# Performance work log

Hardware: AMD Instinct MI355X
Metric: run time of the kernel (lower is better)

## Reference

```python
import jax, jax.numpy as jnp
import numpy as np

N = 50000      # nodes
E = 800000     # edges (avg degree 16)
IN, HID, OUT = 256, 128, 64
K, ALPHA = 4, 0.0  # APPNPConv(k=4, alpha=0.0)


def setup_inputs() -> dict:
    key = jax.random.key(0)
    ks = jax.random.split(key, 5)
    features = jax.random.normal(ks[0], (N, IN), jnp.float32)
    src = jax.random.randint(ks[1], (E,), 0, N, jnp.int32)
    dst = jax.random.randint(ks[2], (E,), 0, N, jnp.int32)
    W1 = jax.random.normal(ks[3], (IN, HID), jnp.float32) / np.float32(np.sqrt(IN))
    b1 = jnp.zeros((HID,), jnp.float32)
    W3 = jax.random.normal(ks[4], (HID, OUT), jnp.float32) / np.float32(np.sqrt(HID))
    b3 = jnp.zeros((OUT,), jnp.float32)
    return dict(features=features, src=src, dst=dst, W1=W1, b1=b1, W3=W3, b3=b3)


def _sym_norms(src, dst, n):
    # D_out^{-1/2} for source side, D_in^{-1/2} for destination side (DGL norm='both')
    ones = jnp.ones((src.shape[0],), jnp.float32)
    deg_out = jax.ops.segment_sum(ones, src, num_segments=n)
    deg_in = jax.ops.segment_sum(ones, dst, num_segments=n)
    return jnp.clip(deg_out, 1.0) ** -0.5, jnp.clip(deg_in, 1.0) ** -0.5


def _prop(x, src, dst, norm_src, norm_dst):
    # x: [N, D]. Symmetric-normalized SpMM: D_in^{-1/2} A D_out^{-1/2} x
    msg = (x * norm_src[:, None])[src]                       # [E, D] gather
    agg = jax.ops.segment_sum(msg, dst, num_segments=x.shape[0])  # [N, D] scatter-add
    return agg * norm_dst[:, None]


def reference(features, src, dst, W1, b1, W3, b3):
    ns, nd = _sym_norms(src, dst, N)
    # GraphConv 1 (weight-first since in_dim > hidden_dim; math identical either way)
    h = _prop(features @ W1, src, dst, ns, nd) + b1
    # dropout is identity in eval mode (training=False)
    # APPNPConv: k=4 power-iteration steps with teleport alpha=0.0
    h0 = h
    for _ in range(K):
        h = (1.0 - ALPHA) * _prop(h, src, dst, ns, nd) + ALPHA * h0
    # GraphConv 3
    out = _prop(h @ W3, src, dst, ns, nd) + b3
    return out
```

## Files before the change

kernel.cpp:

```cpp
#include <hip/hip_runtime.h>
#include <math.h>

#define N_NODES 50000
#define N_EDGES 800000
#define DIN 256
#define DHID 128
#define DOUT 64
#define CSTRIDE 64
#define ZROW N_NODES
#define HBLOCKS 128
#define HCHUNK (N_EDGES / HBLOCKS)
#define HWORDS (N_NODES / 4)
#define SLICE ((size_t)(N_NODES + 1) * 16)
#define NGROUPS (N_NODES / 4)
#define P2BLOCKS 196

#define SB_SENT 3125
#define SB_HS (SB_SENT + HBLOCKS)
#define SB_HD (SB_HS + HBLOCKS)
#define SB_TOT (SB_HD + 66)

__global__ void k_setup(const int* __restrict__ src, const int* __restrict__ dst,
                        unsigned int* __restrict__ pS, unsigned int* __restrict__ pD,
                        unsigned int* __restrict__ csr32,
                        const float* __restrict__ W1, const float* __restrict__ b1,
                        const float* __restrict__ W3,
                        float* __restrict__ W13, float* __restrict__ bb,
                        float* __restrict__ Y0, float* __restrict__ Y1) {
    __shared__ unsigned int h[HWORDS];
    int bx = blockIdx.x, t = threadIdx.x;
    if (bx < SB_SENT) {
        unsigned int v = (unsigned int)ZROW | ((unsigned int)ZROW << 16);
        uint2 o; o.x = v; o.y = v;
        ((uint2*)csr32)[bx * 256 + t] = o;
        return;
    }
    if (bx < SB_HD) {
        const int* idx = (bx < SB_HS) ? src : dst;
        unsigned int* outp = (bx < SB_HS) ? pS : pD;
        int hb = bx - ((bx < SB_HS) ? SB_SENT : SB_HS);
        for (int w = t; w < HWORDS; w += 256) h[w] = 0u;
        __syncthreads();
        int base = hb * HCHUNK;
        for (int i = t; i < HCHUNK; i += 256) {
            int s = idx[base + i];
            atomicAdd(&h[s >> 2], 1u << ((s & 3) << 3));
        }
        __syncthreads();
        outp += (size_t)hb * HWORDS;
        for (int w = t; w < HWORDS; w += 256) outp[w] = h[w];
        return;
    }
    int vb = bx - SB_HD;
    if (vb == 65) {
        if (t < 64) {
            int qq = t >> 4, c2 = t & 15;
            Y0[(size_t)qq * SLICE + ((size_t)ZROW << 4) + c2] = 0.f;
        } else if (t < 128) {
            int t2 = t - 64;
            int qq = t2 >> 4, c2 = t2 & 15;
            Y1[(size_t)qq * SLICE + ((size_t)ZROW << 4) + c2] = 0.f;
        }
        return;
    }
    if (vb == 64) {
        if (t < DOUT) {
            float s = 0.f;
            for (int k = 0; k < DHID; ++k) s += b1[k] * W3[k * DOUT + t];
            bb[t] = s;
        }
        return;
    }
    int idx2 = vb * 256 + t;
    int i = idx2 >> 6, j = idx2 & 63;
    float s = 0.f;
    for (int k = 0; k < DHID; ++k) s += W1[i * DHID + k] * W3[k * DOUT + j];
    W13[idx2] = s;
}

__global__ void k_hpre(const unsigned int* __restrict__ pS,
                       const unsigned int* __restrict__ pD,
                       unsigned int* __restrict__ prefix,
                       float* __restrict__ ns, float* __restrict__ nd,
                       float* __restrict__ cc, int* __restrict__ mG) {
    __shared__ unsigned int sdw[64][4];
    __shared__ unsigned int sow[64][4];
    int t = threadIdx.x;
    int col = t >> 2, sub = t & 3;
    int wid = blockIdx.x * 64 + col;
    bool act = wid < HWORDS;
    unsigned int vals[32];
    unsigned int ps = 0, pd = 0;
    int b0 = sub << 5;
    if (act) {
#pragma unroll
        for (int k = 0; k < 32; ++k) {
            ps += pS[(size_t)(b0 + k) * HWORDS + wid];
            unsigned int w = pD[(size_t)(b0 + k) * HWORDS + wid];
            vals[k] = w;
            pd += w;
        }
    }
    sdw[col][sub] = pd;
    sow[col][sub] = ps;
    __syncthreads();
    if (act) {
        unsigned int base = 0;
        for (int k = 0; k < sub; ++k) base += sdw[col][k];
        unsigned int run = base;
#pragma unroll
        for (int k = 0; k < 32; ++k) {
            prefix[(size_t)(b0 + k) * HWORDS + wid] = run;
            run += vals[k];
        }
        if (sub == 0) {
            unsigned int totd = sdw[col][0] + sdw[col][1] + sdw[col][2] + sdw[col][3];
            unsigned int toto = sow[col][0] + sow[col][1] + sow[col][2] + sow[col][3];
            unsigned int di[4] = {totd & 0xffu, (totd >> 8) & 0xffu,
                                  (totd >> 16) & 0xffu, totd >> 24};
            unsigned int dov[4] = {toto & 0xffu, (toto >> 8) & 0xffu,
                                   (toto >> 16) & 0xffu, toto >> 24};
            float4 vns, vnd, vcc;
            float* pns = &vns.x; float* pnd = &vnd.x; float* pcc = &vcc.x;
            unsigned int mx = 0;
#pragma unroll
            for (int q = 0; q < 4; ++q) {
                if (di[q] > mx) mx = di[q];
                unsigned int a = dov[q] < 1u ? 1u : dov[q];
                unsigned int b = di[q] < 1u ? 1u : di[q];
                float fa = 1.0f / sqrtf((float)a);
                float fb = 1.0f / sqrtf((float)b);
                pns[q] = fa; pnd[q] = fb; pcc[q] = fa * fb;
            }
            *(float4*)(ns + (wid << 2)) = vns;
            *(float4*)(nd + (wid << 2)) = vnd;
            *(float4*)(cc + (wid << 2)) = vcc;
            int m = ((int)mx + 7) & ~7;
            mG[wid] = m > 64 ? 64 : m;
        }
    }
}

__global__ void k_fill(const int* __restrict__ src, const int* __restrict__ dst,
                       const unsigned int* __restrict__ prefix,
                       unsigned short* __restrict__ csr) {
    __shared__ unsigned int h[HWORDS];
    int t = threadIdx.x;
    const unsigned int* prow = prefix + (size_t)blockIdx.x * HWORDS;
    for (int w = t; w < HWORDS; w += 256) h[w] = prow[w];
    __syncthreads();
    int base = blockIdx.x * HCHUNK;
    for (int i = t; i < HCHUNK; i += 256) {
        int s = src[base + i], d = dst[base + i];
        int sh = (d & 3) << 3;
        unsigned int old = atomicAdd(&h[d >> 2], 1u << sh);
        int slot = (int)((old >> sh) & 0xffu);
        csr[((size_t)d << 6) + slot] = (unsigned short)s;
    }
}

__global__ void k_gemm(const float* __restrict__ X, const float* __restrict__ W13,
                       const float* __restrict__ ns, float* __restrict__ Y) {
    __shared__ float As[16][68];
    __shared__ float Bs[16][64];
    int tid = threadIdx.x;
    int tx = tid & 15, ty = tid >> 4;
    int row0 = blockIdx.x * 64;
    float acc[4][4];
#pragma unroll
    for (int i = 0; i < 4; ++i)
#pragma unroll
        for (int j = 0; j < 4; ++j) acc[i][j] = 0.f;

    int lr = tid >> 2;
    int lk = (tid & 3) << 2;
    int arow = row0 + lr;
    if (arow > N_NODES - 1) arow = N_NODES - 1;

    for (int k0 = 0; k0 < DIN; k0 += 16) {
        float4 a = *(const float4*)(X + (size_t)arow * DIN + k0 + lk);
        As[lk + 0][lr] = a.x; As[lk + 1][lr] = a.y;
        As[lk + 2][lr] = a.z; As[lk + 3][lr] = a.w;
        float4 b = *(const float4*)(W13 + (size_t)(k0 + (tid >> 4)) * DOUT + ((tid & 15) << 2));
        *(float4*)&Bs[tid >> 4][(tid & 15) << 2] = b;
        __syncthreads();
#pragma unroll
        for (int k = 0; k < 16; ++k) {
            float4 av = *(const float4*)&As[k][ty << 2];
            float4 bv = *(const float4*)&Bs[k][tx << 2];
            float ar[4] = {av.x, av.y, av.z, av.w};
            float br[4] = {bv.x, bv.y, bv.z, bv.w};
#pragma unroll
            for (int i = 0; i < 4; ++i)
#pragma unroll
                for (int j = 0; j < 4; ++j) acc[i][j] += ar[i] * br[j];
        }
        __syncthreads();
    }
    int qq = tx >> 2;
    int co = (tx & 3) << 2;
#pragma unroll
    for (int i = 0; i < 4; ++i) {
        int row = row0 + (ty << 2) + i;
        if (row < N_NODES) {
            float nsr = ns[row];
            float4 o;
            o.x = acc[i][0] * nsr; o.y = acc[i][1] * nsr;
            o.z = acc[i][2] * nsr; o.w = acc[i][3] * nsr;
            *(float4*)(Y + (size_t)qq * SLICE + ((size_t)row << 4) + co) = o;
        }
    }
}


template <int MODE>
__launch_bounds__(256, 8)
__global__ void k_spmm(const float* __restrict__ xs, float* __restrict__ ys,
                       const unsigned short* __restrict__ csr,
                       const int* __restrict__ mG,
                       const float* __restrict__ cc, const float* __restrict__ ns,
                       const float* __restrict__ nd,
                       const float* __restrict__ bb, const float* __restrict__ b3) {
    __shared__ unsigned short rows[4][256];
    int wid  = threadIdx.x >> 6;
    int lane = threadIdx.x & 63;
    int q    = (blockIdx.x & 7) >> 1;
    int half = blockIdx.x & 1;
    int g    = (blockIdx.x >> 3) * 8 + wid * 2 + half;
    if (g >= NGROUPS) return;
    int node0 = g << 2;

    int nn = lane >> 4, sl = lane & 15;
    const uint2* crow = (const uint2*)(csr + ((size_t)(node0 + nn) << 6)) + sl;
    uint2 rv = *crow;
    unsigned short* bp = &rows[wid][(sl << 4) + nn];
    bp[0]  = (unsigned short)(rv.x & 0xffffu);
    bp[4]  = (unsigned short)(rv.x >> 16);
    bp[8]  = (unsigned short)(rv.y & 0xffffu);
    bp[12] = (unsigned short)(rv.y >> 16);

    int m = __builtin_amdgcn_readfirstlane(mG[g]);

    int n = lane >> 4, e = (lane >> 2) & 3, c4 = lane & 3;
    const unsigned short* rd = &rows[wid][(e << 2) + n];
    const float* xq = xs + (size_t)q * SLICE + (c4 << 2);

    float ax = 0.f, ay = 0.f, az = 0.f, aw = 0.f;
#define LDV(T) const float4 v##T = *(const float4*)(xq + ((size_t)rd[16 * (T)] << 4))
#define ACCV(T) ax += v##T.x; ay += v##T.y; az += v##T.z; aw += v##T.w
    if (m <= 8) {
        LDV(0); LDV(1);
        ACCV(0); ACCV(1);
    } else if (m <= 16) {
        LDV(0); LDV(1); LDV(2); LDV(3);
        ACCV(0); ACCV(1); ACCV(2); ACCV(3);
    } else if (m <= 24) {
        LDV(0); LDV(1); LDV(2); LDV(3); LDV(4); LDV(5);
        ACCV(0); ACCV(1); ACCV(2); ACCV(3); ACCV(4); ACCV(5);
    } else if (m <= 32) {
        LDV(0); LDV(1); LDV(2); LDV(3); LDV(4); LDV(5); LDV(6); LDV(7);
        ACCV(0); ACCV(1); ACCV(2); ACCV(3); ACCV(4); ACCV(5); ACCV(6); ACCV(7);
    } else {
        for (int j2 = 0; j2 < m; j2 += 8) {
            int o = j2 << 2;
            const float4 a = *(const float4*)(xq + ((size_t)rd[o] << 4));
            const float4 b = *(const float4*)(xq + ((size_t)rd[o + 16] << 4));
            ax += a.x; ay += a.y; az += a.z; aw += a.w;
            ax += b.x; ay += b.y; az += b.z; aw += b.w;
        }
    }
#undef LDV
#undef ACCV
    ax += __shfl_xor(ax, 4);  ay += __shfl_xor(ay, 4);
    az += __shfl_xor(az, 4);  aw += __shfl_xor(aw, 4);
    ax += __shfl_xor(ax, 8);  ay += __shfl_xor(ay, 8);
    az += __shfl_xor(az, 8);  aw += __shfl_xor(aw, 8);

    int nodeL = node0 + n;
    int colq  = (q << 4) + (c4 << 2);
    float4 r;
    if (MODE == 0) {
        float cv = cc[nodeL], nv = ns[nodeL];
        float4 bv = *(const float4*)(bb + colq);
        r.x = cv * ax + nv * bv.x; r.y = cv * ay + nv * bv.y;
        r.z = cv * az + nv * bv.z; r.w = cv * aw + nv * bv.w;
    } else if (MODE == 1) {
        float cv = cc[nodeL];
        r.x = cv * ax; r.y = cv * ay; r.z = cv * az; r.w = cv * aw;
    } else {
        float dv = nd[nodeL];
        float4 bv = *(const float4*)(b3 + colq);
        r.x = dv * ax + bv.x; r.y = dv * ay + bv.y;
        r.z = dv * az + bv.z; r.w = dv * aw + bv.w;
    }
    if (e == 0) {
        if (MODE == 2) {
            *(float4*)(ys + ((size_t)nodeL << 6) + colq) = r;
        } else {
            *(float4*)(ys + (size_t)q * SLICE + ((size_t)nodeL << 4) + (c4 << 2)) = r;
        }
    }
}


extern "C" void kernel_launch(void* const* d_in, const int* in_sizes, int n_in,
                              void* d_out, int out_size, void* d_ws, size_t ws_size,
                              hipStream_t stream) {
    const float* X   = (const float*)d_in[0];
    const int*   src = (const int*)d_in[1];
    const int*   dst = (const int*)d_in[2];
    const float* W1  = (const float*)d_in[3];
    const float* b1  = (const float*)d_in[4];
    const float* W3  = (const float*)d_in[5];
    const float* b3  = (const float*)d_in[6];
    float* out = (float*)d_out;

    char* ws = (char*)d_ws;
    size_t off = 0;
    auto alloc = [&](size_t bytes) -> void* {
        void* p = ws + off;
        off = (off + bytes + 255) & ~(size_t)255;
        return p;
    };
    unsigned int*   pS   = (unsigned int*)alloc((size_t)HBLOCKS * HWORDS * 4);
    unsigned int*   pD   = (unsigned int*)alloc((size_t)HBLOCKS * HWORDS * 4);
    unsigned int*   pref = (unsigned int*)alloc((size_t)HBLOCKS * HWORDS * 4);
    float*          Y0   = (float*)alloc(SLICE * 4 * 4);
    float*          Y1   = (float*)alloc(SLICE * 4 * 4);
    unsigned short* csr  = (unsigned short*)alloc((size_t)N_NODES * CSTRIDE * 2);
    float*          ns   = (float*)alloc((size_t)N_NODES * 4);
    float*          nd   = (float*)alloc((size_t)N_NODES * 4);
    float*          cc   = (float*)alloc((size_t)N_NODES * 4);
    int*            mG   = (int*)alloc((size_t)NGROUPS * 4);
    float*          W13  = (float*)alloc((size_t)DIN * DOUT * 4);
    float*          bb   = (float*)alloc(DOUT * 4);

    const int sblk = 1563 * 8;

    k_setup<<<SB_TOT, 256, 0, stream>>>(src, dst, pS, pD, (unsigned int*)csr,
                                        W1, b1, W3, W13, bb, Y0, Y1);
    k_hpre<<<P2BLOCKS, 256, 0, stream>>>(pS, pD, pref, ns, nd, cc, mG);
    k_fill<<<HBLOCKS, 256, 0, stream>>>(src, dst, pref, csr);
    k_gemm<<<(N_NODES + 63) / 64, 256, 0, stream>>>(X, W13, ns, Y0);

    k_spmm<0><<<sblk, 256, 0, stream>>>(Y0, Y1, csr, mG, cc, ns, nd, bb, b3);
    k_spmm<1><<<sblk, 256, 0, stream>>>(Y1, Y0, csr, mG, cc, ns, nd, bb, b3);
    k_spmm<1><<<sblk, 256, 0, stream>>>(Y0, Y1, csr, mG, cc, ns, nd, bb, b3);
    k_spmm<1><<<sblk, 256, 0, stream>>>(Y1, Y0, csr, mG, cc, ns, nd, bb, b3);
    k_spmm<1><<<sblk, 256, 0, stream>>>(Y0, Y1, csr, mG, cc, ns, nd, bb, b3);
    k_spmm<2><<<sblk, 256, 0, stream>>>(Y1, out, csr, mG, cc, ns, nd, bb, b3);
}
```

Baseline: 293.5 us.

## Merge CSR fill and feature GEMM into one launch with 512-thread blocks

The CSR fill kernel and the X·W13 GEMM are combined into a single kernel. Block index picks the role: the first 128 blocks fill the CSR and the rest compute GEMM tiles, now 128 rows per block with 512 threads. This removes one launch and lets the two independent phases run at the same time. Both roles share a dynamic LDS allocation sized for the fill histogram (50 KB), which may reduce occupancy for the GEMM blocks.

```diff
diff --git a/kernel.cpp b/kernel.cpp
--- a/kernel.cpp
+++ b/kernel.cpp
@@ -141,53 +141,62 @@
     }
 }
 
-__global__ void k_fill(const int* __restrict__ src, const int* __restrict__ dst,
-                       const unsigned int* __restrict__ prefix,
-                       unsigned short* __restrict__ csr) {
-    __shared__ unsigned int h[HWORDS];
-    int t = threadIdx.x;
-    const unsigned int* prow = prefix + (size_t)blockIdx.x * HWORDS;
-    for (int w = t; w < HWORDS; w += 256) h[w] = prow[w];
-    __syncthreads();
-    int base = blockIdx.x * HCHUNK;
-    for (int i = t; i < HCHUNK; i += 256) {
-        int s = src[base + i], d = dst[base + i];
-        int sh = (d & 3) << 3;
-        unsigned int old = atomicAdd(&h[d >> 2], 1u << sh);
-        int slot = (int)((old >> sh) & 0xffu);
-        csr[((size_t)d << 6) + slot] = (unsigned short)s;
-    }
-}
-
-__global__ void k_gemm(const float* __restrict__ X, const float* __restrict__ W13,
-                       const float* __restrict__ ns, float* __restrict__ Y) {
-    __shared__ float As[16][68];
-    __shared__ float Bs[16][64];
-    int tid = threadIdx.x;
-    int tx = tid & 15, ty = tid >> 4;
-    int row0 = blockIdx.x * 64;
+#define MB_FILL 128
+#define MB_GEMM 391
+#define MB_TOT (MB_FILL + MB_GEMM)
+#define MID_LDS (HWORDS * 4)
+
+__global__ void k_mid(const int* __restrict__ src, const int* __restrict__ dst,
+                      const unsigned int* __restrict__ prefix,
+                      unsigned short* __restrict__ csr,
+                      const float* __restrict__ X, const float* __restrict__ W13,
+                      const float* __restrict__ ns, float* __restrict__ Y) {
+    extern __shared__ char smem[];
+    int bx = blockIdx.x, t = threadIdx.x;
+    if (bx < MB_FILL) {
+        unsigned int* h = (unsigned int*)smem;
+        const unsigned int* prow = prefix + (size_t)bx * HWORDS;
+        for (int w = t; w < HWORDS; w += 512) h[w] = prow[w];
+        __syncthreads();
+        int base = bx * HCHUNK;
+        for (int i = t; i < HCHUNK; i += 512) {
+            int s = src[base + i], d = dst[base + i];
+            int sh = (d & 3) << 3;
+            unsigned int old = atomicAdd(&h[d >> 2], 1u << sh);
+            int slot = (int)((old >> sh) & 0xffu);
+            csr[((size_t)d << 6) + slot] = (unsigned short)s;
+        }
+        return;
+    }
+    float* As = (float*)smem;
+    float* Bs = (float*)smem + 16 * 132;
+    int gb = bx - MB_FILL;
+    int row0 = gb * 128;
+    int tx = t & 15, ty = t >> 4;
     float acc[4][4];
 #pragma unroll
     for (int i = 0; i < 4; ++i)
 #pragma unroll
         for (int j = 0; j < 4; ++j) acc[i][j] = 0.f;
 
-    int lr = tid >> 2;
-    int lk = (tid & 3) << 2;
+    int lr = t >> 2;
+    int lk = (t & 3) << 2;
     int arow = row0 + lr;
     if (arow > N_NODES - 1) arow = N_NODES - 1;
 
     for (int k0 = 0; k0 < DIN; k0 += 16) {
         float4 a = *(const float4*)(X + (size_t)arow * DIN + k0 + lk);
-        As[lk + 0][lr] = a.x; As[lk + 1][lr] = a.y;
-        As[lk + 2][lr] = a.z; As[lk + 3][lr] = a.w;
-        float4 b = *(const float4*)(W13 + (size_t)(k0 + (tid >> 4)) * DOUT + ((tid & 15) << 2));
-        *(float4*)&Bs[tid >> 4][(tid & 15) << 2] = b;
+        As[(lk + 0) * 132 + lr] = a.x; As[(lk + 1) * 132 + lr] = a.y;
+        As[(lk + 2) * 132 + lr] = a.z; As[(lk + 3) * 132 + lr] = a.w;
+        if (t < 256) {
+            float4 b = *(const float4*)(W13 + (size_t)(k0 + (t >> 4)) * DOUT + ((t & 15) << 2));
+            *(float4*)(Bs + (t >> 4) * 64 + ((t & 15) << 2)) = b;
+        }
         __syncthreads();
 #pragma unroll
         for (int k = 0; k < 16; ++k) {
-            float4 av = *(const float4*)&As[k][ty << 2];
-            float4 bv = *(const float4*)&Bs[k][tx << 2];
+            float4 av = *(const float4*)(As + k * 132 + (ty << 2));
+            float4 bv = *(const float4*)(Bs + k * 64 + (tx << 2));
             float ar[4] = {av.x, av.y, av.z, av.w};
             float br[4] = {bv.x, bv.y, bv.z, bv.w};
 #pragma unroll
@@ -340,8 +349,7 @@
     k_setup<<<SB_TOT, 256, 0, stream>>>(src, dst, pS, pD, (unsigned int*)csr,
                                         W1, b1, W3, W13, bb, Y0, Y1);
     k_hpre<<<P2BLOCKS, 256, 0, stream>>>(pS, pD, pref, ns, nd, cc, mG);
-    k_fill<<<HBLOCKS, 256, 0, stream>>>(src, dst, pref, csr);
-    k_gemm<<<(N_NODES + 63) / 64, 256, 0, stream>>>(X, W13, ns, Y0);
+    k_mid<<<MB_TOT, 512, MID_LDS, stream>>>(src, dst, pref, csr, X, W13, ns, Y0);
 
     k_spmm<0><<<sblk, 256, 0, stream>>>(Y0, Y1, csr, mG, cc, ns, nd, bb, b3);
     k_spmm<1><<<sblk, 256, 0, stream>>>(Y1, Y0, csr, mG, cc, ns, nd, bb, b3);
```

Result: faster. 287.5 us (-2.0%).
